# Kernel optimization log

Hardware: AMD Instinct MI355X
Metric: run time of the kernel (lower is better)

## Reference

```python
import jax, jax.numpy as jnp
import numpy as np


def setup_inputs() -> dict:
    key = jax.random.key(0)
    k1, k2 = jax.random.split(key)
    b, n, d = 4, 4096, 512
    m = 4096
    l = max(n, m)
    x = jax.random.normal(k1, (b, n, d), dtype=jnp.float32)
    t = jax.random.normal(k2, (1, 2 * l - 2, d), dtype=jnp.float32)
    return {"x": x, "t": t, "m": m}


def reference(x, t, m):
    # x: (b, n, d); t: (1, 2*max(n,m)-2, d); output: (b, m, d)
    n = x.shape[1]
    l = max(n, m)
    fft_len = 2 * l
    x_fft = jnp.fft.rfft(x, fft_len, axis=-2)   # (b, l+1, d) complex
    t_fft = jnp.fft.rfft(t, fft_len, axis=-2)   # (1, l+1, d) complex
    o = jnp.fft.irfft(x_fft * t_fft, fft_len, axis=-2)[:, :m]
    return o
```

## Files before the change

kernel.cpp:

```cpp
#include <hip/hip_runtime.h>
#include <math.h>

#define N_FFT   8192
#define SEQ     4096
#define NCH     512
#define TLEN    8190

__device__ __forceinline__ float2 cmul(float2 a, float2 b) {
    return make_float2(a.x * b.x - a.y * b.y, a.x * b.y + a.y * b.x);
}
__device__ __forceinline__ float2 cmulj(float2 a, float2 b) {
    return make_float2(a.x * b.x + a.y * b.y, a.y * b.x - a.x * b.y);
}
__device__ __forceinline__ float2 cadd(float2 a, float2 b) {
    return make_float2(a.x + b.x, a.y + b.y);
}
__device__ __forceinline__ float2 csub(float2 a, float2 b) {
    return make_float2(a.x - b.x, a.y - b.y);
}

constexpr float W32C[16] = {
    1.0f, 0.9807852804032304f, 0.9238795325112867f, 0.8314696123025452f,
    0.7071067811865476f, 0.5555702330196023f, 0.3826834323650898f, 0.1950903220161283f,
    0.0f, -0.1950903220161282f, -0.3826834323650897f, -0.5555702330196020f,
    -0.7071067811865475f, -0.8314696123025453f, -0.9238795325112867f, -0.9807852804032304f
};
constexpr float W32S[16] = {
    -0.0f, -0.1950903220161283f, -0.3826834323650898f, -0.5555702330196022f,
    -0.7071067811865476f, -0.8314696123025452f, -0.9238795325112867f, -0.9807852804032304f,
    -1.0f, -0.9807852804032304f, -0.9238795325112867f, -0.8314696123025453f,
    -0.7071067811865476f, -0.5555702330196022f, -0.3826834323650899f, -0.1950903220161286f
};

constexpr int BREV5[32] = {0,16,8,24,4,20,12,28,2,18,10,26,6,22,14,30,
                           1,17,9,25,5,21,13,29,3,19,11,27,7,23,15,31};
constexpr int BREV4[16] = {0,8,4,12,2,10,6,14,1,9,5,13,3,11,7,15};

__device__ __forceinline__ int brev3i(int b) {
    return ((b & 1) << 2) | (b & 2) | ((b & 4) >> 2);
}

__device__ __forceinline__ void fft32_dif(float2 a[32]) {
#pragma unroll
    for (int s = 4; s >= 0; --s) {
        const int h = 1 << s;
#pragma unroll
        for (int g = 0; g < 32; g += 2 * h) {
#pragma unroll
            for (int i = 0; i < h; ++i) {
                float2 x0 = a[g + i], x1 = a[g + i + h];
                a[g + i] = cadd(x0, x1);
                float2 w = make_float2(W32C[i << (4 - s)], W32S[i << (4 - s)]);
                a[g + i + h] = cmul(csub(x0, x1), w);
            }
        }
    }
}

__device__ __forceinline__ void fft16_dif(float2 a[16]) {
#pragma unroll
    for (int s = 3; s >= 0; --s) {
        const int h = 1 << s;
#pragma unroll
        for (int g = 0; g < 16; g += 2 * h) {
#pragma unroll
            for (int i = 0; i < h; ++i) {
                float2 x0 = a[g + i], x1 = a[g + i + h];
                a[g + i] = cadd(x0, x1);
                float2 w = make_float2(W32C[i << (4 - s)], W32S[i << (4 - s)]);
                a[g + i + h] = cmul(csub(x0, x1), w);
            }
        }
    }
}

__device__ __forceinline__ void ifft16_dit(float2 a[16]) {
#pragma unroll
    for (int s = 0; s <= 3; ++s) {
        const int h = 1 << s;
#pragma unroll
        for (int g = 0; g < 16; g += 2 * h) {
#pragma unroll
            for (int i = 0; i < h; ++i) {
                float2 w = make_float2(W32C[i << (4 - s)], -W32S[i << (4 - s)]);
                float2 t = cmul(a[g + i + h], w);
                float2 x0 = a[g + i];
                a[g + i] = cadd(x0, t);
                a[g + i + h] = csub(x0, t);
            }
        }
    }
}

__device__ __forceinline__ void fft8_dif(float2 a[8]) {
#pragma unroll
    for (int s = 2; s >= 0; --s) {
        const int h = 1 << s;
#pragma unroll
        for (int g = 0; g < 8; g += 2 * h) {
#pragma unroll
            for (int i = 0; i < h; ++i) {
                float2 x0 = a[g + i], x1 = a[g + i + h];
                a[g + i] = cadd(x0, x1);
                int e = (i << (2 - s)) << 2;
                float2 w = make_float2(W32C[e], W32S[e]);
                a[g + i + h] = cmul(csub(x0, x1), w);
            }
        }
    }
}

__device__ __forceinline__ int SLOT(int r, int c) {
    return (r << 8) + (c ^ ((c >> 4) & 7) ^ ((r & 1) << 3));
}
__device__ __forceinline__ int ZADDR(int q) {
    return SLOT(q & 31, (((q >> 5) & 31) << 3) + brev3i((q >> 10) & 7));
}
__device__ __forceinline__ int SLOT16(int r, int c) {
    return (r << 8) + (c ^ ((c >> 4) & 7) ^ ((r & 1) << 3));
}

__global__ __launch_bounds__(256) void twiddle_init(float2* __restrict__ tw) {
    int k = blockIdx.x * 256 + threadIdx.x;
    double th = -2.0 * 3.14159265358979323846 * (double)k / (double)N_FFT;
    tw[k] = make_float2((float)cos(th), (float)sin(th));
}

__global__ __launch_bounds__(256) void transpose_in(const float* __restrict__ x,
                                                    const float* __restrict__ t,
                                                    float2* __restrict__ xT,
                                                    float2* __restrict__ tT) {
    __shared__ float tX[64][65], tY[64][65];
    const int tid = threadIdx.x;
    if (blockIdx.x < 1024) {
        const int bid = blockIdx.x;
        const int pb = bid >> 9;
        const int dt = (bid >> 6) & 7;
        const int nt = bid & 63;
        const int d0 = dt << 6, n0 = nt << 6;
        const float* x0 = x + (size_t)(2 * pb) * SEQ * NCH;
        const float* x1 = x0 + (size_t)SEQ * NCH;
        {
            const int c4 = tid & 15, r16 = tid >> 4;
#pragma unroll
            for (int it = 0; it < 4; ++it) {
                int row = r16 + (it << 4);
                size_t off = (size_t)(n0 + row) * NCH + d0 + (c4 << 2);
                float4 v0 = *(const float4*)(x0 + off);
                float4 v1 = *(const float4*)(x1 + off);
                tX[row][(c4 << 2) + 0] = v0.x; tX[row][(c4 << 2) + 1] = v0.y;
                tX[row][(c4 << 2) + 2] = v0.z; tX[row][(c4 << 2) + 3] = v0.w;
                tY[row][(c4 << 2) + 0] = v1.x; tY[row][(c4 << 2) + 1] = v1.y;
                tY[row][(c4 << 2) + 2] = v1.z; tY[row][(c4 << 2) + 3] = v1.w;
            }
        }
        __syncthreads();
        {
            const int nc = tid & 63, dr4 = tid >> 6;
#pragma unroll
            for (int it = 0; it < 16; ++it) {
                int dr = dr4 + (it << 2);
                xT[(((size_t)(pb * NCH + d0 + dr)) << 12) + n0 + nc] =
                    make_float2(tX[nc][dr], tY[nc][dr]);
            }
        }
    } else {
        const int bid = blockIdx.x - 1024;
        const int nt = bid >> 2, dpt = bid & 3;
        const int n0 = nt << 6, dp0 = dpt << 6;
        {
            const int c = tid & 63, r4 = tid >> 6;
#pragma unroll
            for (int it = 0; it < 16; ++it) {
                int row = r4 + (it << 2);
                int nn = n0 + row;
                float2 v = make_float2(0.f, 0.f);
                if (nn < TLEN)
                    v = *(const float2*)(t + (size_t)nn * NCH + ((dp0 + c) << 1));
                tX[row][c] = v.x;
                tY[row][c] = v.y;
            }
        }
        __syncthreads();
        {
            const int nc = tid & 63, dr4 = tid >> 6;
#pragma unroll
            for (int it = 0; it < 16; ++it) {
                int dr = dr4 + (it << 2);
                tT[(((size_t)(dp0 + dr)) << 13) + n0 + nc] =
                    make_float2(tX[nc][dr], tY[nc][dr]);
            }
        }
    }
}

__global__ __launch_bounds__(256) void tfft3_kernel(const float2* __restrict__ tT,
                                                    const float2* __restrict__ tw,
                                                    float2* __restrict__ Tc) {
    __shared__ float2 z[N_FFT];
    const int tid = threadIdx.x;
    const int d0 = blockIdx.x * 2;
    const int d1 = d0 + 1;
    const float2* tp = tT + ((size_t)blockIdx.x << 13);

    float2 a[32];
#pragma unroll
    for (int n1 = 0; n1 < 32; ++n1)
        a[n1] = tp[(n1 << 8) + tid];
    fft32_dif(a);
    {
        float2 w = tw[tid], w2 = cmul(w, w);
        float2 we = make_float2(1.f, 0.f), wo = w;
#pragma unroll
        for (int k1 = 0; k1 < 32; k1 += 2) {
            z[SLOT(k1, tid)]     = (k1 == 0) ? a[0] : cmul(a[BREV5[k1]], we);
            z[SLOT(k1 + 1, tid)] = cmul(a[BREV5[k1 + 1]], wo);
            we = cmul(we, w2); wo = cmul(wo, w2);
        }
    }
    __syncthreads();

    {
        const int r = tid >> 3, n2p = tid & 7;
#pragma unroll
        for (int n1p = 0; n1p < 32; ++n1p)
            a[n1p] = z[SLOT(r, (n1p << 3) + n2p)];
        fft32_dif(a);
        float2 wb = tw[n2p << 5], wb2 = cmul(wb, wb);
        float2 be = make_float2(1.f, 0.f), bo = wb;
#pragma unroll
        for (int k1p = 0; k1p < 32; k1p += 2) {
            z[SLOT(r, (k1p << 3) + n2p)]       = (k1p == 0) ? a[0] : cmul(a[BREV5[k1p]], be);
            z[SLOT(r, ((k1p + 1) << 3) + n2p)] = cmul(a[BREV5[k1p + 1]], bo);
            be = cmul(be, wb2); bo = cmul(bo, wb2);
        }
    }
    __syncthreads();

#pragma unroll
    for (int u = 0; u < 4; ++u) {
        int f = tid + (u << 8);
        int k1 = f >> 5, k1p = f & 31;
        float2 b[8];
#pragma unroll
        for (int e = 0; e < 8; ++e) b[e] = z[SLOT(k1, (k1p << 3) + e)];
        fft8_dif(b);
#pragma unroll
        for (int j = 0; j < 8; ++j) z[SLOT(k1, (k1p << 3) + j)] = b[j];
    }
    __syncthreads();

    const float sc = 0.5f / (float)N_FFT;
#pragma unroll
    for (int v = 0; v < 16; ++v) {
        int p = tid + (v << 8);
        int q   = p >> 9;
        int rem = p & 511;
        int t_  = rem >> 1, e = rem & 1;
        int j_  = (q << 1) + e;
        int kp  = (t_ >> 4) + ((t_ & 15) << 4) + (BREV4[j_] << 8);
#pragma unroll
        for (int par = 0; par < 2; ++par) {
            int k  = 2 * kp + par;
            int km = (N_FFT - k) & (N_FFT - 1);
            float2 A = z[ZADDR(k)];
            float2 B = z[ZADDR(km)];
            float2 Bj = make_float2(B.x, -B.y);
            float2 T0 = make_float2((A.x + Bj.x) * sc, (A.y + Bj.y) * sc);
            float2 dd = csub(A, Bj);
            float2 T1 = make_float2(dd.y * sc, -dd.x * sc);
            Tc[(size_t)d0 * N_FFT + (par << 12) + p] = T0;
            Tc[(size_t)d1 * N_FFT + (par << 12) + p] = T1;
        }
    }
}

__global__ __launch_bounds__(256, 2) void conv6_kernel(float2* __restrict__ xoT,
                                                       const float2* __restrict__ tw,
                                                       const float2* __restrict__ Tc) {
    __shared__ float2 z[SEQ];
    __shared__ float2 zx[1024];
    const int t = threadIdx.x;
    const int sb = (blockIdx.x & 7) * 128 + (blockIdx.x >> 3);
    const int d  = sb >> 1;
    const int pb = sb & 1;
    float2* xp  = xoT + ((size_t)(pb * NCH + d) << 12);

    float2 a[16], ie[12];

#pragma unroll
    for (int par = 0; par < 2; ++par) {
        if (par == 0) {
#pragma unroll
            for (int n1 = 0; n1 < 16; ++n1)
                a[n1] = xp[(n1 << 8) + t];
        } else {
#pragma unroll
            for (int n1 = 0; n1 < 16; ++n1)
                a[n1] = cmul(xp[(n1 << 8) + t], tw[(n1 << 8) + t]);
        }
        fft16_dif(a);
        {
            float2 w = tw[2 * t];
            float2 w2 = cmul(w, w);
            float2 we = make_float2(1.f, 0.f), wo = w;
#pragma unroll
            for (int k1 = 0; k1 < 16; k1 += 2) {
                z[SLOT16(k1, t)]     = (k1 == 0) ? a[0] : cmul(a[BREV4[k1]], we);
                z[SLOT16(k1 + 1, t)] = cmul(a[BREV4[k1 + 1]], wo);
                we = cmul(we, w2); wo = cmul(wo, w2);
            }
        }
        __syncthreads();

        {
            const int k1 = t >> 4, n3 = t & 15;
#pragma unroll
            for (int n2 = 0; n2 < 16; ++n2)
                a[n2] = z[SLOT16(k1, (n2 << 4) + n3)];
            fft16_dif(a);
            float2 wb = tw[n3 << 5];
            float2 wb2 = cmul(wb, wb);
            float2 be = make_float2(1.f, 0.f), bo = wb;
#pragma unroll
            for (int r1 = 0; r1 < 16; r1 += 2) {
                z[SLOT16(k1, (r1 << 4) + n3)]       = (r1 == 0) ? a[0] : cmul(a[BREV4[r1]], be);
                z[SLOT16(k1, ((r1 + 1) << 4) + n3)] = cmul(a[BREV4[r1 + 1]], bo);
                be = cmul(be, wb2); bo = cmul(bo, wb2);
            }
        }
        __builtin_amdgcn_sched_barrier(0);

        {
            const int k1 = t >> 4, r1 = t & 15;
#pragma unroll
            for (int n3 = 0; n3 < 16; ++n3)
                a[n3] = z[SLOT16(k1, (r1 << 4) + n3)];
            fft16_dif(a);
            const float4* tp = (const float4*)(Tc + ((size_t)d << 13) + (par << 12));
#pragma unroll
            for (int q = 0; q < 8; ++q) {
                float4 f4 = tp[(q << 8) + t];
                a[2 * q]     = cmul(a[2 * q],     make_float2(f4.x, f4.y));
                a[2 * q + 1] = cmul(a[2 * q + 1], make_float2(f4.z, f4.w));
            }
            ifft16_dit(a);
#pragma unroll
            for (int n3 = 0; n3 < 16; ++n3)
                z[SLOT16(k1, (r1 << 4) + n3)] = a[n3];
        }
        __builtin_amdgcn_sched_barrier(0);

        {
            const int k1 = t >> 4, n3 = t & 15;
            float2 wb = tw[n3 << 5], wb2 = cmul(wb, wb);
            float2 be = make_float2(1.f, 0.f), bo = wb;
#pragma unroll
            for (int r1 = 0; r1 < 16; r1 += 2) {
                float2 v0 = z[SLOT16(k1, (r1 << 4) + n3)];
                float2 v1 = z[SLOT16(k1, ((r1 + 1) << 4) + n3)];
                a[BREV4[r1]]     = (r1 == 0) ? v0 : cmulj(v0, be);
                a[BREV4[r1 + 1]] = cmulj(v1, bo);
                be = cmul(be, wb2); bo = cmul(bo, wb2);
            }
            ifft16_dit(a);
#pragma unroll
            for (int n2 = 0; n2 < 16; ++n2)
                z[SLOT16(k1, (n2 << 4) + n3)] = a[n2];
        }
        __syncthreads();

        {
            float2 w = tw[2 * t], w2 = cmul(w, w);
            float2 we = make_float2(1.f, 0.f), wo = w;
#pragma unroll
            for (int k1 = 0; k1 < 16; k1 += 2) {
                float2 v0 = z[SLOT16(k1, t)];
                float2 v1 = z[SLOT16(k1 + 1, t)];
                a[BREV4[k1]]     = (k1 == 0) ? v0 : cmulj(v0, we);
                a[BREV4[k1 + 1]] = cmulj(v1, wo);
                we = cmul(we, w2); wo = cmul(wo, w2);
            }
            ifft16_dit(a);
        }

        if (par == 0) {
#pragma unroll
            for (int n1 = 0; n1 < 12; ++n1) ie[n1] = a[n1];
#pragma unroll
            for (int n1 = 12; n1 < 16; ++n1)
                zx[((n1 - 12) << 8) + t] = a[n1];
        } else {
#pragma unroll
            for (int n1 = 0; n1 < 12; ++n1) {
                int n = (n1 << 8) + t;
                xp[n] = cadd(ie[n1], cmulj(a[n1], tw[n]));
            }
#pragma unroll
            for (int n1 = 12; n1 < 16; ++n1) {
                int n = (n1 << 8) + t;
                float2 ue = zx[((n1 - 12) << 8) + t];
                xp[n] = cadd(ue, cmulj(a[n1], tw[n]));
            }
        }
    }
}

__global__ __launch_bounds__(256) void transpose_out(const float2* __restrict__ oT,
                                                     float* __restrict__ out) {
    __shared__ float2 tile[32][65];
    const int tid = threadIdx.x;
    const int bid = blockIdx.x;
    const int pb = bid >> 10;
    const int dt = (bid >> 6) & 15;
    const int nt = bid & 63;
    const int d0 = dt << 5, n0 = nt << 6;

    {
        const int nl = tid & 63, dl = tid >> 6;
#pragma unroll
        for (int i = 0; i < 8; ++i) {
            int dd = dl + (i << 2);
            tile[dd][nl] = oT[(((size_t)(pb * NCH + d0 + dd)) << 12) + n0 + nl];
        }
    }
    __syncthreads();
    {
        const int dl = tid & 31, ns = tid >> 5;
        float* o0 = out + (size_t)(2 * pb) * SEQ * NCH;
        float* o1 = o0 + (size_t)SEQ * NCH;
#pragma unroll
        for (int j = 0; j < 8; ++j) {
            int nn = n0 + ns + (j << 3);
            float2 v = tile[dl][ns + (j << 3)];
            o0[(size_t)nn * NCH + d0 + dl] = v.x;
            o1[(size_t)nn * NCH + d0 + dl] = v.y;
        }
    }
}

__global__ __launch_bounds__(256) void tfft2_kernel(const float* __restrict__ t,
                                                    const float2* __restrict__ tw,
                                                    float2* __restrict__ Tc) {
    __shared__ float2 z[N_FFT];
    const int tid = threadIdx.x;
    const int d0 = blockIdx.x * 2;
    const int d1 = d0 + 1;

    float2 a[32];
#pragma unroll
    for (int n1 = 0; n1 < 32; ++n1) {
        int n = (n1 << 8) + tid;
        float va = 0.f, vb = 0.f;
        if (n < TLEN) {
            va = t[(size_t)n * NCH + d0];
            vb = t[(size_t)n * NCH + d1];
        }
        a[n1] = make_float2(va, vb);
    }
    fft32_dif(a);
    {
        float2 w = tw[tid], w2 = cmul(w, w);
        float2 we = make_float2(1.f, 0.f), wo = w;
#pragma unroll
        for (int k1 = 0; k1 < 32; k1 += 2) {
            z[SLOT(k1, tid)]     = (k1 == 0) ? a[0] : cmul(a[BREV5[k1]], we);
            z[SLOT(k1 + 1, tid)] = cmul(a[BREV5[k1 + 1]], wo);
            we = cmul(we, w2); wo = cmul(wo, w2);
        }
    }
    __syncthreads();
    {
        const int r = tid >> 3, n2p = tid & 7;
#pragma unroll
        for (int n1p = 0; n1p < 32; ++n1p)
            a[n1p] = z[SLOT(r, (n1p << 3) + n2p)];
        fft32_dif(a);
        float2 wb = tw[n2p << 5], wb2 = cmul(wb, wb);
        float2 be = make_float2(1.f, 0.f), bo = wb;
#pragma unroll
        for (int k1p = 0; k1p < 32; k1p += 2) {
            z[SLOT(r, (k1p << 3) + n2p)]       = (k1p == 0) ? a[0] : cmul(a[BREV5[k1p]], be);
            z[SLOT(r, ((k1p + 1) << 3) + n2p)] = cmul(a[BREV5[k1p + 1]], bo);
            be = cmul(be, wb2); bo = cmul(bo, wb2);
        }
    }
    __syncthreads();
#pragma unroll
    for (int u = 0; u < 4; ++u) {
        int f = tid + (u << 8);
        int k1 = f >> 5, k1p = f & 31;
        float2 b[8];
#pragma unroll
        for (int e = 0; e < 8; ++e) b[e] = z[SLOT(k1, (k1p << 3) + e)];
        fft8_dif(b);
#pragma unroll
        for (int j = 0; j < 8; ++j) z[SLOT(k1, (k1p << 3) + j)] = b[j];
    }
    __syncthreads();

    const float sc = 0.5f / (float)N_FFT;
#pragma unroll
    for (int v = 0; v < 16; ++v) {
        int s = tid + (v << 8);
        int k1 = s >> 8, r1 = (s >> 4) & 15, j = s & 15;
        int kp = k1 + (r1 << 4) + (BREV4[j] << 8);
#pragma unroll
        for (int par = 0; par < 2; ++par) {
            int k  = 2 * kp + par;
            int km = (N_FFT - k) & (N_FFT - 1);
            float2 A = z[ZADDR(k)];
            float2 B = z[ZADDR(km)];
            float2 Bj = make_float2(B.x, -B.y);
            float2 T0 = make_float2((A.x + Bj.x) * sc, (A.y + Bj.y) * sc);
            float2 dd = csub(A, Bj);
            float2 T1 = make_float2(dd.y * sc, -dd.x * sc);
            Tc[(size_t)d0 * N_FFT + (par << 12) + s] = T0;
            Tc[(size_t)d1 * N_FFT + (par << 12) + s] = T1;
        }
    }
}

template<bool OT>
__global__ __launch_bounds__(256, 2) void conv3_kernel(const float* __restrict__ x,
                                                       const float2* __restrict__ tw,
                                                       const float2* __restrict__ Tc,
                                                       float2* __restrict__ oT,
                                                       float* __restrict__ out) {
    __shared__ float2 z[SEQ];
    const int tid = threadIdx.x;
    const int sb = (blockIdx.x & 7) * 128 + (blockIdx.x >> 3);
    const int d  = sb >> 1;
    const int pb = sb & 1;

    const float* x0 = x + (size_t)(2 * pb) * SEQ * NCH + d;
    const float* x1 = x0 + (size_t)SEQ * NCH;

    float2 a[16], ie[16];

#pragma unroll
    for (int par = 0; par < 2; ++par) {
        if (par == 1) __syncthreads();

        if (par == 0) {
#pragma unroll
            for (int n1 = 0; n1 < 16; ++n1) {
                int n = (n1 << 8) + tid;
                a[n1] = make_float2(x0[(size_t)n * NCH], x1[(size_t)n * NCH]);
            }
        } else {
#pragma unroll
            for (int n1 = 0; n1 < 16; ++n1) {
                int n = (n1 << 8) + tid;
                float2 v = make_float2(x0[(size_t)n * NCH], x1[(size_t)n * NCH]);
                a[n1] = cmul(v, tw[n]);
            }
        }
        fft16_dif(a);
        {
            float2 w = tw[2 * tid], w2 = cmul(w, w);
            float2 we = make_float2(1.f, 0.f), wo = w;
#pragma unroll
            for (int k1 = 0; k1 < 16; k1 += 2) {
                z[SLOT16(k1, tid)]     = (k1 == 0) ? a[0] : cmul(a[BREV4[k1]], we);
                z[SLOT16(k1 + 1, tid)] = cmul(a[BREV4[k1 + 1]], wo);
                we = cmul(we, w2); wo = cmul(wo, w2);
            }
        }
        __syncthreads();
        {
            const int k1 = tid >> 4, n3 = tid & 15;
#pragma unroll
            for (int n2 = 0; n2 < 16; ++n2)
                a[n2] = z[SLOT16(k1, (n2 << 4) + n3)];
            fft16_dif(a);
            float2 wb = tw[n3 << 5], wb2 = cmul(wb, wb);
            float2 be = make_float2(1.f, 0.f), bo = wb;
#pragma unroll
            for (int r1 = 0; r1 < 16; r1 += 2) {
                z[SLOT16(k1, (r1 << 4) + n3)]       = (r1 == 0) ? a[0] : cmul(a[BREV4[r1]], be);
                z[SLOT16(k1, ((r1 + 1) << 4) + n3)] = cmul(a[BREV4[r1 + 1]], bo);
                be = cmul(be, wb2); bo = cmul(bo, wb2);
            }
        }
        __syncthreads();
        {
            const int k1 = tid >> 4, r1 = tid & 15;
#pragma unroll
            for (int n3 = 0; n3 < 16; ++n3)
                a[n3] = z[SLOT16(k1, (r1 << 4) + n3)];
            fft16_dif(a);
            const float2* Td = Tc + ((size_t)d << 13) + (par << 12);
#pragma unroll
            for (int j = 0; j < 16; ++j) {
                float2 T = Td[((tid >> 4) << 8) + ((tid & 15) << 4) + j];
                a[j] = cmul(a[j], T);
            }
            ifft16_dit(a);
#pragma unroll
            for (int n3 = 0; n3 < 16; ++n3)
                z[SLOT16(k1, (r1 << 4) + n3)] = a[n3];
        }
        __syncthreads();
        {
            const int k1 = tid >> 4, n3 = tid & 15;
            float2 wb = tw[n3 << 5], wb2 = cmul(wb, wb);
            float2 be = make_float2(1.f, 0.f), bo = wb;
#pragma unroll
            for (int r1 = 0; r1 < 16; r1 += 2) {
                float2 v0 = z[SLOT16(k1, (r1 << 4) + n3)];
                float2 v1 = z[SLOT16(k1, ((r1 + 1) << 4) + n3)];
                a[BREV4[r1]]     = (r1 == 0) ? v0 : cmulj(v0, be);
                a[BREV4[r1 + 1]] = cmulj(v1, bo);
                be = cmul(be, wb2); bo = cmul(bo, wb2);
            }
            ifft16_dit(a);
#pragma unroll
            for (int n2 = 0; n2 < 16; ++n2)
                z[SLOT16(k1, (n2 << 4) + n3)] = a[n2];
        }
        __syncthreads();
        {
            float2 w = tw[2 * tid], w2 = cmul(w, w);
            float2 we = make_float2(1.f, 0.f), wo = w;
#pragma unroll
            for (int k1 = 0; k1 < 16; k1 += 2) {
                float2 v0 = z[SLOT16(k1, tid)];
                float2 v1 = z[SLOT16(k1 + 1, tid)];
                a[BREV4[k1]]     = (k1 == 0) ? v0 : cmulj(v0, we);
                a[BREV4[k1 + 1]] = cmulj(v1, wo);
                we = cmul(we, w2); wo = cmul(wo, w2);
            }
            ifft16_dit(a);
        }

        if (par == 0) {
#pragma unroll
            for (int n1 = 0; n1 < 16; ++n1) ie[n1] = a[n1];
        } else {
            if constexpr (OT) {
                float2* op = oT + (((size_t)(pb * NCH + d)) << 12);
#pragma unroll
                for (int n1 = 0; n1 < 16; ++n1) {
                    int n = (n1 << 8) + tid;
                    op[n] = cadd(ie[n1], cmulj(a[n1], tw[n]));
                }
            } else {
                float* o0 = out + (size_t)(2 * pb) * SEQ * NCH + d;
                float* o1 = o0 + (size_t)SEQ * NCH;
#pragma unroll
                for (int n1 = 0; n1 < 16; ++n1) {
                    int n = (n1 << 8) + tid;
                    float2 o = cadd(ie[n1], cmulj(a[n1], tw[n]));
                    o0[(size_t)n * NCH] = o.x;
                    o1[(size_t)n * NCH] = o.y;
                }
            }
        }
    }
}

extern "C" void kernel_launch(void* const* d_in, const int* in_sizes, int n_in,
                              void* d_out, int out_size, void* d_ws, size_t ws_size,
                              hipStream_t stream) {
    (void)in_sizes; (void)n_in; (void)out_size;
    const float* x = (const float*)d_in[0];
    const float* t = (const float*)d_in[1];
    float* out = (float*)d_out;

    float2* tw  = (float2*)d_ws;
    float2* Tc  = tw + N_FFT;
    float2* xoT = Tc + (size_t)NCH * N_FFT;
    float2* tT  = xoT + 2ull * NCH * SEQ;

    const size_t need_full = sizeof(float2) * ((size_t)N_FFT + (size_t)NCH * N_FFT
                                               + 2ull * NCH * SEQ
                                               + 256ull * N_FFT);
    const size_t need_ot   = sizeof(float2) * ((size_t)N_FFT + (size_t)NCH * N_FFT
                                               + 2ull * NCH * SEQ);

    twiddle_init<<<N_FFT / 256, 256, 0, stream>>>(tw);
    if (ws_size >= need_full) {
        transpose_in<<<1536, 256, 0, stream>>>(x, t, xoT, tT);
        tfft3_kernel<<<NCH / 2, 256, 0, stream>>>(tT, tw, Tc);
        conv6_kernel<<<1024, 256, 0, stream>>>(xoT, tw, Tc);
        transpose_out<<<2048, 256, 0, stream>>>(xoT, out);
    } else if (ws_size >= need_ot) {
        tfft2_kernel<<<NCH / 2, 256, 0, stream>>>(t, tw, Tc);
        conv3_kernel<true><<<1024, 256, 0, stream>>>(x, tw, Tc, xoT, out);
        transpose_out<<<2048, 256, 0, stream>>>(xoT, out);
    } else {
        tfft2_kernel<<<NCH / 2, 256, 0, stream>>>(t, tw, Tc);
        conv3_kernel<false><<<1024, 256, 0, stream>>>(x, tw, Tc, nullptr, out);
    }
}
```

Before: 92.85 us.

## Fold twiddle init into transpose, hand-unroll radix-16 butterflies, prefetch filter spectrum

Twiddle generation moves into extra blocks of the input transpose kernel, which removes one kernel launch on the main path. The radix-16 forward and inverse FFTs are written out as explicit butterflies, so trivial twiddles (1 and -j) skip the complex multiply. The filter-spectrum loads in conv6 are issued earlier, before the shared-memory passes, to hide their global-memory latency, at the cost of holding eight float4 values in registers longer, which may raise register pressure.

After: 83.36 us. 1.11x faster.

```diff
diff --git a/kernel.cpp b/kernel.cpp
--- a/kernel.cpp
+++ b/kernel.cpp
@@ -40,6 +40,25 @@
     return ((b & 1) << 2) | (b & 2) | ((b & 4) >> 2);
 }
 
+template<int E>
+__device__ __forceinline__ void bfly_dif(float2& x0, float2& x1) {
+    float2 s = csub(x0, x1);
+    x0 = cadd(x0, x1);
+    if constexpr (E == 0)       x1 = s;
+    else if constexpr (E == 8)  x1 = make_float2(s.y, -s.x);
+    else                        x1 = cmul(s, make_float2(W32C[E], W32S[E]));
+}
+template<int E>
+__device__ __forceinline__ void bfly_dit(float2& x0, float2& x1) {
+    float2 t;
+    if constexpr (E == 0)       t = x1;
+    else if constexpr (E == 8)  t = make_float2(-x1.y, x1.x);
+    else                        t = cmulj(x1, make_float2(W32C[E], W32S[E]));
+    float2 x0o = x0;
+    x0 = cadd(x0o, t);
+    x1 = csub(x0o, t);
+}
+
 __device__ __forceinline__ void fft32_dif(float2 a[32]) {
 #pragma unroll
     for (int s = 4; s >= 0; --s) {
@@ -58,38 +77,41 @@
 }
 
 __device__ __forceinline__ void fft16_dif(float2 a[16]) {
-#pragma unroll
-    for (int s = 3; s >= 0; --s) {
-        const int h = 1 << s;
-#pragma unroll
-        for (int g = 0; g < 16; g += 2 * h) {
-#pragma unroll
-            for (int i = 0; i < h; ++i) {
-                float2 x0 = a[g + i], x1 = a[g + i + h];
-                a[g + i] = cadd(x0, x1);
-                float2 w = make_float2(W32C[i << (4 - s)], W32S[i << (4 - s)]);
-                a[g + i + h] = cmul(csub(x0, x1), w);
-            }
-        }
-    }
+    bfly_dif<0>(a[0],a[8]);   bfly_dif<2>(a[1],a[9]);
+    bfly_dif<4>(a[2],a[10]);  bfly_dif<6>(a[3],a[11]);
+    bfly_dif<8>(a[4],a[12]);  bfly_dif<10>(a[5],a[13]);
+    bfly_dif<12>(a[6],a[14]); bfly_dif<14>(a[7],a[15]);
+    bfly_dif<0>(a[0],a[4]);   bfly_dif<4>(a[1],a[5]);
+    bfly_dif<8>(a[2],a[6]);   bfly_dif<12>(a[3],a[7]);
+    bfly_dif<0>(a[8],a[12]);  bfly_dif<4>(a[9],a[13]);
+    bfly_dif<8>(a[10],a[14]); bfly_dif<12>(a[11],a[15]);
+    bfly_dif<0>(a[0],a[2]);   bfly_dif<8>(a[1],a[3]);
+    bfly_dif<0>(a[4],a[6]);   bfly_dif<8>(a[5],a[7]);
+    bfly_dif<0>(a[8],a[10]);  bfly_dif<8>(a[9],a[11]);
+    bfly_dif<0>(a[12],a[14]); bfly_dif<8>(a[13],a[15]);
+    bfly_dif<0>(a[0],a[1]);   bfly_dif<0>(a[2],a[3]);
+    bfly_dif<0>(a[4],a[5]);   bfly_dif<0>(a[6],a[7]);
+    bfly_dif<0>(a[8],a[9]);   bfly_dif<0>(a[10],a[11]);
+    bfly_dif<0>(a[12],a[13]); bfly_dif<0>(a[14],a[15]);
 }
 
 __device__ __forceinline__ void ifft16_dit(float2 a[16]) {
-#pragma unroll
-    for (int s = 0; s <= 3; ++s) {
-        const int h = 1 << s;
-#pragma unroll
-        for (int g = 0; g < 16; g += 2 * h) {
-#pragma unroll
-            for (int i = 0; i < h; ++i) {
-                float2 w = make_float2(W32C[i << (4 - s)], -W32S[i << (4 - s)]);
-                float2 t = cmul(a[g + i + h], w);
-                float2 x0 = a[g + i];
-                a[g + i] = cadd(x0, t);
-                a[g + i + h] = csub(x0, t);
-            }
-        }
-    }
+    bfly_dit<0>(a[0],a[1]);   bfly_dit<0>(a[2],a[3]);
+    bfly_dit<0>(a[4],a[5]);   bfly_dit<0>(a[6],a[7]);
+    bfly_dit<0>(a[8],a[9]);   bfly_dit<0>(a[10],a[11]);
+    bfly_dit<0>(a[12],a[13]); bfly_dit<0>(a[14],a[15]);
+    bfly_dit<0>(a[0],a[2]);   bfly_dit<8>(a[1],a[3]);
+    bfly_dit<0>(a[4],a[6]);   bfly_dit<8>(a[5],a[7]);
+    bfly_dit<0>(a[8],a[10]);  bfly_dit<8>(a[9],a[11]);
+    bfly_dit<0>(a[12],a[14]); bfly_dit<8>(a[13],a[15]);
+    bfly_dit<0>(a[0],a[4]);   bfly_dit<4>(a[1],a[5]);
+    bfly_dit<8>(a[2],a[6]);   bfly_dit<12>(a[3],a[7]);
+    bfly_dit<0>(a[8],a[12]);  bfly_dit<4>(a[9],a[13]);
+    bfly_dit<8>(a[10],a[14]); bfly_dit<12>(a[11],a[15]);
+    bfly_dit<0>(a[0],a[8]);   bfly_dit<2>(a[1],a[9]);
+    bfly_dit<4>(a[2],a[10]);  bfly_dit<6>(a[3],a[11]);
+    bfly_dit<8>(a[4],a[12]);  bfly_dit<10>(a[5],a[13]);
+    bfly_dit<12>(a[6],a[14]); bfly_dit<14>(a[7],a[15]);
 }
 
 __device__ __forceinline__ void fft8_dif(float2 a[8]) {
@@ -129,9 +151,16 @@
 __global__ __launch_bounds__(256) void transpose_in(const float* __restrict__ x,
                                                     const float* __restrict__ t,
                                                     float2* __restrict__ xT,
-                                                    float2* __restrict__ tT) {
+                                                    float2* __restrict__ tT,
+                                                    float2* __restrict__ tw) {
     __shared__ float tX[64][65], tY[64][65];
     const int tid = threadIdx.x;
+    if (blockIdx.x >= 1536) {
+        int k = (blockIdx.x - 1536) * 256 + tid;
+        double th = -2.0 * 3.14159265358979323846 * (double)k / (double)N_FFT;
+        tw[k] = make_float2((float)cos(th), (float)sin(th));
+        return;
+    }
     if (blockIdx.x < 1024) {
         const int bid = blockIdx.x;
         const int pb = bid >> 9;
@@ -290,6 +319,9 @@
 
 #pragma unroll
     for (int par = 0; par < 2; ++par) {
+        const float4* tp = (const float4*)(Tc + ((size_t)d << 13) + (par << 12));
+        float4 tf0, tf1, tf2, tf3, tf4, tf5, tf6, tf7;
+
         if (par == 0) {
 #pragma unroll
             for (int n1 = 0; n1 < 16; ++n1)
@@ -311,6 +343,7 @@
                 we = cmul(we, w2); wo = cmul(wo, w2);
             }
         }
+        tf0 = tp[t]; tf1 = tp[256 + t]; tf2 = tp[512 + t]; tf3 = tp[768 + t];
         __syncthreads();
 
         {
@@ -329,6 +362,7 @@
                 be = cmul(be, wb2); bo = cmul(bo, wb2);
             }
         }
+        tf4 = tp[1024 + t]; tf5 = tp[1280 + t]; tf6 = tp[1536 + t]; tf7 = tp[1792 + t];
         __builtin_amdgcn_sched_barrier(0);
 
         {
@@ -337,13 +371,22 @@
             for (int n3 = 0; n3 < 16; ++n3)
                 a[n3] = z[SLOT16(k1, (r1 << 4) + n3)];
             fft16_dif(a);
-            const float4* tp = (const float4*)(Tc + ((size_t)d << 13) + (par << 12));
-#pragma unroll
-            for (int q = 0; q < 8; ++q) {
-                float4 f4 = tp[(q << 8) + t];
-                a[2 * q]     = cmul(a[2 * q],     make_float2(f4.x, f4.y));
-                a[2 * q + 1] = cmul(a[2 * q + 1], make_float2(f4.z, f4.w));
-            }
+            a[0]  = cmul(a[0],  make_float2(tf0.x, tf0.y));
+            a[1]  = cmul(a[1],  make_float2(tf0.z, tf0.w));
+            a[2]  = cmul(a[2],  make_float2(tf1.x, tf1.y));
+            a[3]  = cmul(a[3],  make_float2(tf1.z, tf1.w));
+            a[4]  = cmul(a[4],  make_float2(tf2.x, tf2.y));
+            a[5]  = cmul(a[5],  make_float2(tf2.z, tf2.w));
+            a[6]  = cmul(a[6],  make_float2(tf3.x, tf3.y));
+            a[7]  = cmul(a[7],  make_float2(tf3.z, tf3.w));
+            a[8]  = cmul(a[8],  make_float2(tf4.x, tf4.y));
+            a[9]  = cmul(a[9],  make_float2(tf4.z, tf4.w));
+            a[10] = cmul(a[10], make_float2(tf5.x, tf5.y));
+            a[11] = cmul(a[11], make_float2(tf5.z, tf5.w));
+            a[12] = cmul(a[12], make_float2(tf6.x, tf6.y));
+            a[13] = cmul(a[13], make_float2(tf6.z, tf6.w));
+            a[14] = cmul(a[14], make_float2(tf7.x, tf7.y));
+            a[15] = cmul(a[15], make_float2(tf7.z, tf7.w));
             ifft16_dit(a);
 #pragma unroll
             for (int n3 = 0; n3 < 16; ++n3)
@@ -679,17 +722,18 @@
     const size_t need_ot   = sizeof(float2) * ((size_t)N_FFT + (size_t)NCH * N_FFT
                                                + 2ull * NCH * SEQ);
 
-    twiddle_init<<<N_FFT / 256, 256, 0, stream>>>(tw);
     if (ws_size >= need_full) {
-        transpose_in<<<1536, 256, 0, stream>>>(x, t, xoT, tT);
+        transpose_in<<<1568, 256, 0, stream>>>(x, t, xoT, tT, tw);
         tfft3_kernel<<<NCH / 2, 256, 0, stream>>>(tT, tw, Tc);
         conv6_kernel<<<1024, 256, 0, stream>>>(xoT, tw, Tc);
         transpose_out<<<2048, 256, 0, stream>>>(xoT, out);
     } else if (ws_size >= need_ot) {
+        twiddle_init<<<N_FFT / 256, 256, 0, stream>>>(tw);
         tfft2_kernel<<<NCH / 2, 256, 0, stream>>>(t, tw, Tc);
         conv3_kernel<true><<<1024, 256, 0, stream>>>(x, tw, Tc, xoT, out);
         transpose_out<<<2048, 256, 0, stream>>>(xoT, out);
     } else {
+        twiddle_init<<<N_FFT / 256, 256, 0, stream>>>(tw);
         tfft2_kernel<<<NCH / 2, 256, 0, stream>>>(t, tw, Tc);
         conv3_kernel<false><<<1024, 256, 0, stream>>>(x, tw, Tc, nullptr, out);
     }
```
